# Kernel tuning notes

Hardware: AMD Instinct MI355X
Metric: run time of the kernel (lower is better)

The kernel has to match this reference:

```python
import jax, jax.numpy as jnp
from jax import lax
import numpy as np

B, T, IN, H, OUT = 8192, 512, 8, 64, 1


def setup_inputs() -> dict:
    key = jax.random.key(0)
    ks = jax.random.split(key, 7)
    s_ih = 1.0 / np.sqrt(H)
    # PyTorch LSTM param layout: gates stacked as [i, f, g, o] along dim 0
    W_ih = jax.random.uniform(ks[0], (4 * H, IN), jnp.float32, -s_ih, s_ih)
    W_hh = jax.random.uniform(ks[1], (4 * H, H), jnp.float32, -s_ih, s_ih)
    b_ih = jax.random.uniform(ks[2], (4 * H,), jnp.float32, -s_ih, s_ih)
    b_hh = jax.random.uniform(ks[3], (4 * H,), jnp.float32, -s_ih, s_ih)
    W_fc = jax.random.uniform(ks[4], (OUT, H), jnp.float32, -s_ih, s_ih)
    b_fc = jax.random.uniform(ks[5], (OUT,), jnp.float32, -s_ih, s_ih)
    x = jax.random.normal(ks[6], (B, T, IN), jnp.float32)
    return {"x": x, "W_ih": W_ih, "W_hh": W_hh, "b_ih": b_ih,
            "b_hh": b_hh, "W_fc": W_fc, "b_fc": b_fc}


def _lstm_last_h(x, W_ih, W_hh, b_ih, b_hh):
    # x: [B, T, IN] -> last hidden state [B, H]
    Bn = x.shape[0]
    Hn = W_hh.shape[1]
    b = b_ih + b_hh  # [4H]

    def step(carry, xt):
        h, c = carry  # [B, H] each
        gates = xt @ W_ih.T + h @ W_hh.T + b  # [B, 4H]
        i, f, g, o = jnp.split(gates, 4, axis=-1)
        i = jax.nn.sigmoid(i)
        f = jax.nn.sigmoid(f)
        g = jnp.tanh(g)
        o = jax.nn.sigmoid(o)
        c = f * c + i * g
        h = o * jnp.tanh(c)
        return (h, c), None

    h0 = jnp.zeros((Bn, Hn), x.dtype)
    c0 = jnp.zeros((Bn, Hn), x.dtype)
    (hT, _), _ = lax.scan(step, (h0, c0), jnp.swapaxes(x, 0, 1))  # scan over T
    return hT


def reference(x, W_ih, W_hh, b_ih, b_hh, W_fc, b_fc):
    hT = _lstm_last_h(x, W_ih, W_hh, b_ih, b_hh)  # [B, H]
    return hT @ W_fc.T + b_fc  # [B, OUT]
```

## Files before the change

kernel.cpp:

```cpp
#include <hip/hip_runtime.h>


typedef _Float16 f16_t;
typedef _Float16 half8 __attribute__((ext_vector_type(8)));
typedef __fp16 fp16x2 __attribute__((ext_vector_type(2)));
typedef float floatx2 __attribute__((ext_vector_type(2)));
typedef float floatx4 __attribute__((ext_vector_type(4)));

#define Bn 8192
#define Tn 512
#define INn 8
#define Hn 64
#define BT 16
#define CHUNK 16
#define NCHUNK (Tn / CHUNK)
#define HSTRIDE 72
#define XTSTRIDE 136

__device__ __forceinline__ floatx2 act_pair(float zi0, float zi1,
                                            float zf0, float zf1,
                                            float zg0, float zg1,
                                            float zo0, float zo1,
                                            floatx2& chat) {
  const floatx2 one  = {1.f, 1.f};
  const float  K2   = 2.8853900817779268f;
  const floatx2 K2v  = {K2, K2};
  const floatx2 mK2v = {-K2, -K2};
  const floatx2 clmp = {126.f, 126.f};
  floatx2 A = {__builtin_amdgcn_exp2f(zi0), __builtin_amdgcn_exp2f(zi1)};
  floatx2 G = {__builtin_amdgcn_exp2f(zg0), __builtin_amdgcn_exp2f(zg1)};
  floatx2 F = {__builtin_amdgcn_exp2f(zf0), __builtin_amdgcn_exp2f(zf1)};
  floatx2 O = {__builtin_amdgcn_exp2f(zo0), __builtin_amdgcn_exp2f(zo1)};
  floatx2 PA  = A + one;
  floatx2 PG  = G + one;
  floatx2 PF  = F + one;
  floatx2 PAG = PA * PG;
  floatx2 num = __builtin_elementwise_fma(G, K2v, mK2v) * PF;
  floatx2 s   = __builtin_elementwise_fma(chat, PAG, num);
  floatx2 P3  = PF * PAG;
  floatx2 R   = {__builtin_amdgcn_rcpf(P3.x), __builtin_amdgcn_rcpf(P3.y)};
  chat = __builtin_elementwise_min(s * R, clmp);
  floatx2 C2 = {__builtin_amdgcn_exp2f(chat.x), __builtin_amdgcn_exp2f(chat.y)};
  floatx2 P4 = (O + one) * (C2 + one);
  floatx2 Rh = {__builtin_amdgcn_rcpf(P4.x), __builtin_amdgcn_rcpf(P4.y)};
  return (C2 - one) * Rh;
}

__global__ __launch_bounds__(256, 2)
void lstm_fused(const float* __restrict__ xg,
                const float* __restrict__ W_ih,
                const float* __restrict__ W_hh,
                const float* __restrict__ b_ih,
                const float* __restrict__ b_hh,
                const float* __restrict__ W_fc,
                const float* __restrict__ b_fc,
                float* __restrict__ out)
{
  __shared__ alignas(16) f16_t hbuf[2][BT][HSTRIDE];
  __shared__ alignas(16) f16_t xlds[2][CHUNK][XTSTRIDE];

  const int tid   = threadIdx.x;
  const int wv    = tid >> 6;
  const int lane  = tid & 63;
  const int n     = lane & 15;
  const int q     = lane >> 4;
  const int bbase = blockIdx.x * BT;

  const float LOG2E = 1.4426950408889634f;

  half8 bf[4][3];
  #pragma unroll
  for (int g = 0; g < 4; ++g) {
    const float sc = (g == 2) ? (2.f * LOG2E) : (-LOG2E);
    const int C = g * 64 + wv * 16 + n;
    #pragma unroll
    for (int c = 0; c < 3; ++c) {
      half8 v;
      #pragma unroll
      for (int j = 0; j < 8; ++j) {
        const int k = c * 32 + q * 8 + j;
        float w = 0.f;
        if (k < Hn)            w = W_hh[C * Hn + k] * sc;
        else if (k < Hn + INn) w = W_ih[C * INn + (k - Hn)] * sc;
        v[j] = (f16_t)w;
      }
      bf[g][c] = v;
    }
  }

  const int u = wv * 16 + n;
  const float pb_i = -(b_ih[u]       + b_hh[u])       * LOG2E;
  const float pb_f = -(b_ih[64 + u]  + b_hh[64 + u])  * LOG2E;
  const float pb_g =  (b_ih[128 + u] + b_hh[128 + u]) * (2.f * LOG2E);
  const float pb_o = -(b_ih[192 + u] + b_hh[192 + u]) * LOG2E;
  const floatx4 bi  = {pb_i, pb_i, pb_i, pb_i};
  const floatx4 bfv = {pb_f, pb_f, pb_f, pb_f};
  const floatx4 bg  = {pb_g, pb_g, pb_g, pb_g};
  const floatx4 bo  = {pb_o, pb_o, pb_o, pb_o};

  for (int i = tid; i < BT * HSTRIDE; i += 256) ((f16_t*)hbuf[0])[i] = (f16_t)0.f;

  const int row_s = tid >> 4;
  const int tt_s  = tid & 15;
  const float* xps = xg + ((size_t)(bbase + row_s) * Tn + tt_s) * INn;

  float4 pa = *(const float4*)(xps);
  float4 pb2 = *(const float4*)(xps + 4);

  floatx2 chat01 = {0.f, 0.f};
  floatx2 chat23 = {0.f, 0.f};

  for (int ch = 0; ch < NCHUNK; ++ch) {
    union { half8 v; fp16x2 h2[4]; } P;
    P.h2[0] = __builtin_amdgcn_cvt_pkrtz(pa.x, pa.y);
    P.h2[1] = __builtin_amdgcn_cvt_pkrtz(pa.z, pa.w);
    P.h2[2] = __builtin_amdgcn_cvt_pkrtz(pb2.x, pb2.y);
    P.h2[3] = __builtin_amdgcn_cvt_pkrtz(pb2.z, pb2.w);
    *(half8*)&xlds[ch & 1][tt_s][row_s * 8] = P.v;
    __syncthreads();

    const int chn = (ch + 1 < NCHUNK) ? (ch + 1) : 0;
    pa  = *(const float4*)(xps + (size_t)chn * CHUNK * INn);
    pb2 = *(const float4*)(xps + (size_t)chn * CHUNK * INn + 4);

    #pragma unroll
    for (int tt = 0; tt < CHUNK; ++tt) {
      const int p  = tt & 1;
      const int pn = p ^ 1;

      const half8 a0 = *(const half8*)&hbuf[p][n][q * 8];
      const half8 a1 = *(const half8*)&hbuf[p][n][32 + q * 8];
      const half8 a2 = *(const half8*)&xlds[ch & 1][tt][n * 8];

      floatx4 ai = __builtin_amdgcn_mfma_f32_16x16x32_f16(a0, bf[0][0], bi, 0, 0, 0);
      ai = __builtin_amdgcn_mfma_f32_16x16x32_f16(a1, bf[0][1], ai, 0, 0, 0);
      ai = __builtin_amdgcn_mfma_f32_16x16x32_f16(a2, bf[0][2], ai, 0, 0, 0);
      floatx4 af = __builtin_amdgcn_mfma_f32_16x16x32_f16(a0, bf[1][0], bfv, 0, 0, 0);
      af = __builtin_amdgcn_mfma_f32_16x16x32_f16(a1, bf[1][1], af, 0, 0, 0);
      af = __builtin_amdgcn_mfma_f32_16x16x32_f16(a2, bf[1][2], af, 0, 0, 0);
      floatx4 ag = __builtin_amdgcn_mfma_f32_16x16x32_f16(a0, bf[2][0], bg, 0, 0, 0);
      ag = __builtin_amdgcn_mfma_f32_16x16x32_f16(a1, bf[2][1], ag, 0, 0, 0);
      ag = __builtin_amdgcn_mfma_f32_16x16x32_f16(a2, bf[2][2], ag, 0, 0, 0);
      floatx4 ao = __builtin_amdgcn_mfma_f32_16x16x32_f16(a0, bf[3][0], bo, 0, 0, 0);
      ao = __builtin_amdgcn_mfma_f32_16x16x32_f16(a1, bf[3][1], ao, 0, 0, 0);
      ao = __builtin_amdgcn_mfma_f32_16x16x32_f16(a2, bf[3][2], ao, 0, 0, 0);

      const floatx2 h01 = act_pair(ai[0], ai[1], af[0], af[1],
                                   ag[0], ag[1], ao[0], ao[1], chat01);
      const floatx2 h23 = act_pair(ai[2], ai[3], af[2], af[3],
                                   ag[2], ag[3], ao[2], ao[3], chat23);

      hbuf[pn][q * 4 + 0][u] = (f16_t)h01.x;
      hbuf[pn][q * 4 + 1][u] = (f16_t)h01.y;
      hbuf[pn][q * 4 + 2][u] = (f16_t)h23.x;
      hbuf[pn][q * 4 + 3][u] = (f16_t)h23.y;

      __syncthreads();
    }
  }

  if (tid < 64) {
    const int b = lane & 15;
    const int part = lane >> 4;
    float s = 0.f;
    #pragma unroll
    for (int k = 0; k < 16; ++k) {
      const int uu = part * 16 + k;
      s = __builtin_fmaf((float)hbuf[0][b][uu], W_fc[uu], s);
    }
    s += __shfl_down(s, 32);
    s += __shfl_down(s, 16);
    if (lane < 16) out[bbase + b] = s + b_fc[0];
  }
}

extern "C" void kernel_launch(void* const* d_in, const int* in_sizes, int n_in,
                              void* d_out, int out_size, void* d_ws, size_t ws_size,
                              hipStream_t stream) {
  const float* x    = (const float*)d_in[0];
  const float* W_ih = (const float*)d_in[1];
  const float* W_hh = (const float*)d_in[2];
  const float* b_ih = (const float*)d_in[3];
  const float* b_hh = (const float*)d_in[4];
  const float* W_fc = (const float*)d_in[5];
  const float* b_fc = (const float*)d_in[6];
  float* out = (float*)d_out;
  dim3 grid(Bn / BT), block(256);
  hipLaunchKernelGGL(lstm_fused, grid, block, 0, stream,
                     x, W_ih, W_hh, b_ih, b_hh, W_fc, b_fc, out);
}
```

Baseline: 448.3 us.

## Precompute next-step input projection off the recurrent critical path and remove per-chunk barrier

Result: slower. 462.3 us (+3.1%).

```diff
diff --git a/kernel.cpp b/kernel.cpp
--- a/kernel.cpp
+++ b/kernel.cpp
@@ -104,25 +104,31 @@
   const int tt_s  = tid & 15;
   const float* xps = xg + ((size_t)(bbase + row_s) * Tn + tt_s) * INn;
 
-  float4 pa = *(const float4*)(xps);
-  float4 pb2 = *(const float4*)(xps + 4);
+  {
+    float4 a  = *(const float4*)(xps);
+    float4 b2 = *(const float4*)(xps + 4);
+    union { half8 v; fp16x2 h2[4]; } P;
+    P.h2[0] = __builtin_amdgcn_cvt_pkrtz(a.x, a.y);
+    P.h2[1] = __builtin_amdgcn_cvt_pkrtz(a.z, a.w);
+    P.h2[2] = __builtin_amdgcn_cvt_pkrtz(b2.x, b2.y);
+    P.h2[3] = __builtin_amdgcn_cvt_pkrtz(b2.z, b2.w);
+    *(half8*)&xlds[0][tt_s][row_s * 8] = P.v;
+  }
+  float4 pa  = *(const float4*)(xps + CHUNK * INn);
+  float4 pb2 = *(const float4*)(xps + CHUNK * INn + 4);
+
+  __syncthreads();
+
+  half8 a2 = *(const half8*)&xlds[0][0][n * 8];
+  floatx4 xi  = __builtin_amdgcn_mfma_f32_16x16x32_f16(a2, bf[0][2], bi,  0, 0, 0);
+  floatx4 xfv = __builtin_amdgcn_mfma_f32_16x16x32_f16(a2, bf[1][2], bfv, 0, 0, 0);
+  floatx4 xgv = __builtin_amdgcn_mfma_f32_16x16x32_f16(a2, bf[2][2], bg,  0, 0, 0);
+  floatx4 xo  = __builtin_amdgcn_mfma_f32_16x16x32_f16(a2, bf[3][2], bo,  0, 0, 0);
 
   floatx2 chat01 = {0.f, 0.f};
   floatx2 chat23 = {0.f, 0.f};
 
   for (int ch = 0; ch < NCHUNK; ++ch) {
-    union { half8 v; fp16x2 h2[4]; } P;
-    P.h2[0] = __builtin_amdgcn_cvt_pkrtz(pa.x, pa.y);
-    P.h2[1] = __builtin_amdgcn_cvt_pkrtz(pa.z, pa.w);
-    P.h2[2] = __builtin_amdgcn_cvt_pkrtz(pb2.x, pb2.y);
-    P.h2[3] = __builtin_amdgcn_cvt_pkrtz(pb2.z, pb2.w);
-    *(half8*)&xlds[ch & 1][tt_s][row_s * 8] = P.v;
-    __syncthreads();
-
-    const int chn = (ch + 1 < NCHUNK) ? (ch + 1) : 0;
-    pa  = *(const float4*)(xps + (size_t)chn * CHUNK * INn);
-    pb2 = *(const float4*)(xps + (size_t)chn * CHUNK * INn + 4);
-
     #pragma unroll
     for (int tt = 0; tt < CHUNK; ++tt) {
       const int p  = tt & 1;
@@ -130,30 +136,48 @@
 
       const half8 a0 = *(const half8*)&hbuf[p][n][q * 8];
       const half8 a1 = *(const half8*)&hbuf[p][n][32 + q * 8];
-      const half8 a2 = *(const half8*)&xlds[ch & 1][tt][n * 8];
-
-      floatx4 ai = __builtin_amdgcn_mfma_f32_16x16x32_f16(a0, bf[0][0], bi, 0, 0, 0);
+
+      floatx4 ai = __builtin_amdgcn_mfma_f32_16x16x32_f16(a0, bf[0][0], xi,  0, 0, 0);
+      floatx4 af = __builtin_amdgcn_mfma_f32_16x16x32_f16(a0, bf[1][0], xfv, 0, 0, 0);
+      floatx4 ag = __builtin_amdgcn_mfma_f32_16x16x32_f16(a0, bf[2][0], xgv, 0, 0, 0);
+      floatx4 ao = __builtin_amdgcn_mfma_f32_16x16x32_f16(a0, bf[3][0], xo,  0, 0, 0);
       ai = __builtin_amdgcn_mfma_f32_16x16x32_f16(a1, bf[0][1], ai, 0, 0, 0);
-      ai = __builtin_amdgcn_mfma_f32_16x16x32_f16(a2, bf[0][2], ai, 0, 0, 0);
-      floatx4 af = __builtin_amdgcn_mfma_f32_16x16x32_f16(a0, bf[1][0], bfv, 0, 0, 0);
       af = __builtin_amdgcn_mfma_f32_16x16x32_f16(a1, bf[1][1], af, 0, 0, 0);
-      af = __builtin_amdgcn_mfma_f32_16x16x32_f16(a2, bf[1][2], af, 0, 0, 0);
-      floatx4 ag = __builtin_amdgcn_mfma_f32_16x16x32_f16(a0, bf[2][0], bg, 0, 0, 0);
       ag = __builtin_amdgcn_mfma_f32_16x16x32_f16(a1, bf[2][1], ag, 0, 0, 0);
-      ag = __builtin_amdgcn_mfma_f32_16x16x32_f16(a2, bf[2][2], ag, 0, 0, 0);
-      floatx4 ao = __builtin_amdgcn_mfma_f32_16x16x32_f16(a0, bf[3][0], bo, 0, 0, 0);
       ao = __builtin_amdgcn_mfma_f32_16x16x32_f16(a1, bf[3][1], ao, 0, 0, 0);
-      ao = __builtin_amdgcn_mfma_f32_16x16x32_f16(a2, bf[3][2], ao, 0, 0, 0);
+
+      if (tt == 0) {
+        union { half8 v; fp16x2 h2[4]; } P;
+        P.h2[0] = __builtin_amdgcn_cvt_pkrtz(pa.x, pa.y);
+        P.h2[1] = __builtin_amdgcn_cvt_pkrtz(pa.z, pa.w);
+        P.h2[2] = __builtin_amdgcn_cvt_pkrtz(pb2.x, pb2.y);
+        P.h2[3] = __builtin_amdgcn_cvt_pkrtz(pb2.z, pb2.w);
+        *(half8*)&xlds[(ch + 1) & 1][tt_s][row_s * 8] = P.v;
+      }
+      if (tt == 1) {
+        const int chn = (ch + 2 < NCHUNK) ? (ch + 2) : 0;
+        pa  = *(const float4*)(xps + (size_t)chn * CHUNK * INn);
+        pb2 = *(const float4*)(xps + (size_t)chn * CHUNK * INn + 4);
+      }
 
       const floatx2 h01 = act_pair(ai[0], ai[1], af[0], af[1],
                                    ag[0], ag[1], ao[0], ao[1], chat01);
+      hbuf[pn][q * 4 + 0][u] = (f16_t)h01.x;
+      hbuf[pn][q * 4 + 1][u] = (f16_t)h01.y;
       const floatx2 h23 = act_pair(ai[2], ai[3], af[2], af[3],
                                    ag[2], ag[3], ao[2], ao[3], chat23);
-
-      hbuf[pn][q * 4 + 0][u] = (f16_t)h01.x;
-      hbuf[pn][q * 4 + 1][u] = (f16_t)h01.y;
       hbuf[pn][q * 4 + 2][u] = (f16_t)h23.x;
       hbuf[pn][q * 4 + 3][u] = (f16_t)h23.y;
+
+      {
+        const int nbuf = (tt == CHUNK - 1) ? ((ch + 1) & 1) : (ch & 1);
+        const int ntt  = (tt + 1) & (CHUNK - 1);
+        a2 = *(const half8*)&xlds[nbuf][ntt][n * 8];
+        xi  = __builtin_amdgcn_mfma_f32_16x16x32_f16(a2, bf[0][2], bi,  0, 0, 0);
+        xfv = __builtin_amdgcn_mfma_f32_16x16x32_f16(a2, bf[1][2], bfv, 0, 0, 0);
+        xgv = __builtin_amdgcn_mfma_f32_16x16x32_f16(a2, bf[2][2], bg,  0, 0, 0);
+        xo  = __builtin_amdgcn_mfma_f32_16x16x32_f16(a2, bf[3][2], bo,  0, 0, 0);
+      }
 
       __syncthreads();
     }
```

## Interleave two batch tiles per block to overlap MFMA and activation chains

Applied to the files above, without the earlier changes.

Measured after the change: 517.5 us. +15.4%, slower.

```diff
diff --git a/kernel.cpp b/kernel.cpp
--- a/kernel.cpp
+++ b/kernel.cpp
@@ -12,6 +12,7 @@
 #define INn 8
 #define Hn 64
 #define BT 16
+#define NT 2
 #define CHUNK 16
 #define NCHUNK (Tn / CHUNK)
 #define HSTRIDE 72
@@ -46,7 +47,7 @@
   return (C2 - one) * Rh;
 }
 
-__global__ __launch_bounds__(256, 2)
+__global__ __launch_bounds__(256, 1)
 void lstm_fused(const float* __restrict__ xg,
                 const float* __restrict__ W_ih,
                 const float* __restrict__ W_hh,
@@ -56,15 +57,15 @@
                 const float* __restrict__ b_fc,
                 float* __restrict__ out)
 {
-  __shared__ alignas(16) f16_t hbuf[2][BT][HSTRIDE];
-  __shared__ alignas(16) f16_t xlds[2][CHUNK][XTSTRIDE];
+  __shared__ alignas(16) f16_t hbuf[NT][2][BT][HSTRIDE];
+  __shared__ alignas(16) f16_t xlds[NT][2][CHUNK][XTSTRIDE];
 
   const int tid   = threadIdx.x;
   const int wv    = tid >> 6;
   const int lane  = tid & 63;
   const int n     = lane & 15;
   const int q     = lane >> 4;
-  const int bbase = blockIdx.x * BT;
+  const int bbase = blockIdx.x * (BT * NT);
 
   const float LOG2E = 1.4426950408889634f;
 
@@ -98,79 +99,119 @@
   const floatx4 bg  = {pb_g, pb_g, pb_g, pb_g};
   const floatx4 bo  = {pb_o, pb_o, pb_o, pb_o};
 
-  for (int i = tid; i < BT * HSTRIDE; i += 256) ((f16_t*)hbuf[0])[i] = (f16_t)0.f;
+  for (int i = tid; i < NT * 2 * BT * HSTRIDE; i += 256)
+    ((f16_t*)hbuf)[i] = (f16_t)0.f;
 
   const int row_s = tid >> 4;
   const int tt_s  = tid & 15;
-  const float* xps = xg + ((size_t)(bbase + row_s) * Tn + tt_s) * INn;
-
-  float4 pa = *(const float4*)(xps);
-  float4 pb2 = *(const float4*)(xps + 4);
-
-  floatx2 chat01 = {0.f, 0.f};
-  floatx2 chat23 = {0.f, 0.f};
+  const float* xps0 = xg + ((size_t)(bbase + row_s) * Tn + tt_s) * INn;
+  const float* xps1 = xps0 + (size_t)BT * Tn * INn;
+
+  float4 pa0 = *(const float4*)(xps0);
+  float4 pb0 = *(const float4*)(xps0 + 4);
+  float4 pa1 = *(const float4*)(xps1);
+  float4 pb1 = *(const float4*)(xps1 + 4);
+
+  floatx2 chat01_0 = {0.f, 0.f};
+  floatx2 chat23_0 = {0.f, 0.f};
+  floatx2 chat01_1 = {0.f, 0.f};
+  floatx2 chat23_1 = {0.f, 0.f};
 
   for (int ch = 0; ch < NCHUNK; ++ch) {
-    union { half8 v; fp16x2 h2[4]; } P;
-    P.h2[0] = __builtin_amdgcn_cvt_pkrtz(pa.x, pa.y);
-    P.h2[1] = __builtin_amdgcn_cvt_pkrtz(pa.z, pa.w);
-    P.h2[2] = __builtin_amdgcn_cvt_pkrtz(pb2.x, pb2.y);
-    P.h2[3] = __builtin_amdgcn_cvt_pkrtz(pb2.z, pb2.w);
-    *(half8*)&xlds[ch & 1][tt_s][row_s * 8] = P.v;
+    {
+      union { half8 v; fp16x2 h2[4]; } P;
+      P.h2[0] = __builtin_amdgcn_cvt_pkrtz(pa0.x, pa0.y);
+      P.h2[1] = __builtin_amdgcn_cvt_pkrtz(pa0.z, pa0.w);
+      P.h2[2] = __builtin_amdgcn_cvt_pkrtz(pb0.x, pb0.y);
+      P.h2[3] = __builtin_amdgcn_cvt_pkrtz(pb0.z, pb0.w);
+      *(half8*)&xlds[0][ch & 1][tt_s][row_s * 8] = P.v;
+      P.h2[0] = __builtin_amdgcn_cvt_pkrtz(pa1.x, pa1.y);
+      P.h2[1] = __builtin_amdgcn_cvt_pkrtz(pa1.z, pa1.w);
+      P.h2[2] = __builtin_amdgcn_cvt_pkrtz(pb1.x, pb1.y);
+      P.h2[3] = __builtin_amdgcn_cvt_pkrtz(pb1.z, pb1.w);
+      *(half8*)&xlds[1][ch & 1][tt_s][row_s * 8] = P.v;
+    }
     __syncthreads();
 
     const int chn = (ch + 1 < NCHUNK) ? (ch + 1) : 0;
-    pa  = *(const float4*)(xps + (size_t)chn * CHUNK * INn);
-    pb2 = *(const float4*)(xps + (size_t)chn * CHUNK * INn + 4);
+    pa0 = *(const float4*)(xps0 + (size_t)chn * CHUNK * INn);
+    pb0 = *(const float4*)(xps0 + (size_t)chn * CHUNK * INn + 4);
+    pa1 = *(const float4*)(xps1 + (size_t)chn * CHUNK * INn);
+    pb1 = *(const float4*)(xps1 + (size_t)chn * CHUNK * INn + 4);
 
     #pragma unroll
     for (int tt = 0; tt < CHUNK; ++tt) {
       const int p  = tt & 1;
       const int pn = p ^ 1;
 
-      const half8 a0 = *(const half8*)&hbuf[p][n][q * 8];
-      const half8 a1 = *(const half8*)&hbuf[p][n][32 + q * 8];
-      const half8 a2 = *(const half8*)&xlds[ch & 1][tt][n * 8];
-
-      floatx4 ai = __builtin_amdgcn_mfma_f32_16x16x32_f16(a0, bf[0][0], bi, 0, 0, 0);
-      ai = __builtin_amdgcn_mfma_f32_16x16x32_f16(a1, bf[0][1], ai, 0, 0, 0);
-      ai = __builtin_amdgcn_mfma_f32_16x16x32_f16(a2, bf[0][2], ai, 0, 0, 0);
-      floatx4 af = __builtin_amdgcn_mfma_f32_16x16x32_f16(a0, bf[1][0], bfv, 0, 0, 0);
-      af = __builtin_amdgcn_mfma_f32_16x16x32_f16(a1, bf[1][1], af, 0, 0, 0);
-      af = __builtin_amdgcn_mfma_f32_16x16x32_f16(a2, bf[1][2], af, 0, 0, 0);
-      floatx4 ag = __builtin_amdgcn_mfma_f32_16x16x32_f16(a0, bf[2][0], bg, 0, 0, 0);
-      ag = __builtin_amdgcn_mfma_f32_16x16x32_f16(a1, bf[2][1], ag, 0, 0, 0);
-      ag = __builtin_amdgcn_mfma_f32_16x16x32_f16(a2, bf[2][2], ag, 0, 0, 0);
-      floatx4 ao = __builtin_amdgcn_mfma_f32_16x16x32_f16(a0, bf[3][0], bo, 0, 0, 0);
-      ao = __builtin_amdgcn_mfma_f32_16x16x32_f16(a1, bf[3][1], ao, 0, 0, 0);
-      ao = __builtin_amdgcn_mfma_f32_16x16x32_f16(a2, bf[3][2], ao, 0, 0, 0);
-
-      const floatx2 h01 = act_pair(ai[0], ai[1], af[0], af[1],
-                                   ag[0], ag[1], ao[0], ao[1], chat01);
-      const floatx2 h23 = act_pair(ai[2], ai[3], af[2], af[3],
-                                   ag[2], ag[3], ao[2], ao[3], chat23);
-
-      hbuf[pn][q * 4 + 0][u] = (f16_t)h01.x;
-      hbuf[pn][q * 4 + 1][u] = (f16_t)h01.y;
-      hbuf[pn][q * 4 + 2][u] = (f16_t)h23.x;
-      hbuf[pn][q * 4 + 3][u] = (f16_t)h23.y;
+      const half8 a00 = *(const half8*)&hbuf[0][p][n][q * 8];
+      const half8 a01 = *(const half8*)&hbuf[0][p][n][32 + q * 8];
+      const half8 a02 = *(const half8*)&xlds[0][ch & 1][tt][n * 8];
+      const half8 a10 = *(const half8*)&hbuf[1][p][n][q * 8];
+      const half8 a11 = *(const half8*)&hbuf[1][p][n][32 + q * 8];
+      const half8 a12 = *(const half8*)&xlds[1][ch & 1][tt][n * 8];
+
+      floatx4 ai0 = __builtin_amdgcn_mfma_f32_16x16x32_f16(a00, bf[0][0], bi,  0, 0, 0);
+      floatx4 af0 = __builtin_amdgcn_mfma_f32_16x16x32_f16(a00, bf[1][0], bfv, 0, 0, 0);
+      floatx4 ag0 = __builtin_amdgcn_mfma_f32_16x16x32_f16(a00, bf[2][0], bg,  0, 0, 0);
+      floatx4 ao0 = __builtin_amdgcn_mfma_f32_16x16x32_f16(a00, bf[3][0], bo,  0, 0, 0);
+      floatx4 ai1 = __builtin_amdgcn_mfma_f32_16x16x32_f16(a10, bf[0][0], bi,  0, 0, 0);
+      floatx4 af1 = __builtin_amdgcn_mfma_f32_16x16x32_f16(a10, bf[1][0], bfv, 0, 0, 0);
+      floatx4 ag1 = __builtin_amdgcn_mfma_f32_16x16x32_f16(a10, bf[2][0], bg,  0, 0, 0);
+      floatx4 ao1 = __builtin_amdgcn_mfma_f32_16x16x32_f16(a10, bf[3][0], bo,  0, 0, 0);
+
+      ai0 = __builtin_amdgcn_mfma_f32_16x16x32_f16(a01, bf[0][1], ai0, 0, 0, 0);
+      af0 = __builtin_amdgcn_mfma_f32_16x16x32_f16(a01, bf[1][1], af0, 0, 0, 0);
+      ag0 = __builtin_amdgcn_mfma_f32_16x16x32_f16(a01, bf[2][1], ag0, 0, 0, 0);
+      ao0 = __builtin_amdgcn_mfma_f32_16x16x32_f16(a01, bf[3][1], ao0, 0, 0, 0);
+      ai1 = __builtin_amdgcn_mfma_f32_16x16x32_f16(a11, bf[0][1], ai1, 0, 0, 0);
+      af1 = __builtin_amdgcn_mfma_f32_16x16x32_f16(a11, bf[1][1], af1, 0, 0, 0);
+      ag1 = __builtin_amdgcn_mfma_f32_16x16x32_f16(a11, bf[2][1], ag1, 0, 0, 0);
+      ao1 = __builtin_amdgcn_mfma_f32_16x16x32_f16(a11, bf[3][1], ao1, 0, 0, 0);
+
+      ai0 = __builtin_amdgcn_mfma_f32_16x16x32_f16(a02, bf[0][2], ai0, 0, 0, 0);
+      af0 = __builtin_amdgcn_mfma_f32_16x16x32_f16(a02, bf[1][2], af0, 0, 0, 0);
+      ag0 = __builtin_amdgcn_mfma_f32_16x16x32_f16(a02, bf[2][2], ag0, 0, 0, 0);
+      ao0 = __builtin_amdgcn_mfma_f32_16x16x32_f16(a02, bf[3][2], ao0, 0, 0, 0);
+      ai1 = __builtin_amdgcn_mfma_f32_16x16x32_f16(a12, bf[0][2], ai1, 0, 0, 0);
+      af1 = __builtin_amdgcn_mfma_f32_16x16x32_f16(a12, bf[1][2], af1, 0, 0, 0);
+      ag1 = __builtin_amdgcn_mfma_f32_16x16x32_f16(a12, bf[2][2], ag1, 0, 0, 0);
+      ao1 = __builtin_amdgcn_mfma_f32_16x16x32_f16(a12, bf[3][2], ao1, 0, 0, 0);
+
+      const floatx2 h01_0 = act_pair(ai0[0], ai0[1], af0[0], af0[1],
+                                     ag0[0], ag0[1], ao0[0], ao0[1], chat01_0);
+      hbuf[0][pn][q * 4 + 0][u] = (f16_t)h01_0.x;
+      hbuf[0][pn][q * 4 + 1][u] = (f16_t)h01_0.y;
+      const floatx2 h23_0 = act_pair(ai0[2], ai0[3], af0[2], af0[3],
+                                     ag0[2], ag0[3], ao0[2], ao0[3], chat23_0);
+      hbuf[0][pn][q * 4 + 2][u] = (f16_t)h23_0.x;
+      hbuf[0][pn][q * 4 + 3][u] = (f16_t)h23_0.y;
+      const floatx2 h01_1 = act_pair(ai1[0], ai1[1], af1[0], af1[1],
+                                     ag1[0], ag1[1], ao1[0], ao1[1], chat01_1);
+      hbuf[1][pn][q * 4 + 0][u] = (f16_t)h01_1.x;
+      hbuf[1][pn][q * 4 + 1][u] = (f16_t)h01_1.y;
+      const floatx2 h23_1 = act_pair(ai1[2], ai1[3], af1[2], af1[3],
+                                     ag1[2], ag1[3], ao1[2], ao1[3], chat23_1);
+      hbuf[1][pn][q * 4 + 2][u] = (f16_t)h23_1.x;
+      hbuf[1][pn][q * 4 + 3][u] = (f16_t)h23_1.y;
 
       __syncthreads();
     }
   }
 
-  if (tid < 64) {
+  if (wv < NT) {
+    const int tile = wv;
     const int b = lane & 15;
     const int part = lane >> 4;
     float s = 0.f;
     #pragma unroll
     for (int k = 0; k < 16; ++k) {
       const int uu = part * 16 + k;
-      s = __builtin_fmaf((float)hbuf[0][b][uu], W_fc[uu], s);
+      s = __builtin_fmaf((float)hbuf[tile][0][b][uu], W_fc[uu], s);
     }
     s += __shfl_down(s, 32);
     s += __shfl_down(s, 16);
-    if (lane < 16) out[bbase + b] = s + b_fc[0];
+    if (lane < 16) out[bbase + tile * BT + b] = s + b_fc[0];
   }
 }
 
@@ -185,7 +226,7 @@
   const float* W_fc = (const float*)d_in[5];
   const float* b_fc = (const float*)d_in[6];
   float* out = (float*)d_out;
-  dim3 grid(Bn / BT), block(256);
+  dim3 grid(Bn / (BT * NT)), block(256);
   hipLaunchKernelGGL(lstm_fused, grid, block, 0, stream,
                      x, W_ih, W_hh, b_ih, b_hh, W_fc, b_fc, out);
 }
```

## Transpose LSTM MFMA operands, use 16x16x16 for input term, vectorize h stores

Applied to the files above, without the earlier changes.

Measured after the change: 446.0 us. About the same (-0.5%).

```diff
diff --git a/kernel.cpp b/kernel.cpp
--- a/kernel.cpp
+++ b/kernel.cpp
@@ -3,6 +3,7 @@
 
 typedef _Float16 f16_t;
 typedef _Float16 half8 __attribute__((ext_vector_type(8)));
+typedef _Float16 half4 __attribute__((ext_vector_type(4)));
 typedef __fp16 fp16x2 __attribute__((ext_vector_type(2)));
 typedef float floatx2 __attribute__((ext_vector_type(2)));
 typedef float floatx4 __attribute__((ext_vector_type(4)));
@@ -15,7 +16,7 @@
 #define CHUNK 16
 #define NCHUNK (Tn / CHUNK)
 #define HSTRIDE 72
-#define XTSTRIDE 136
+#define XROW 24
 
 __device__ __forceinline__ floatx2 act_pair(float zi0, float zi1,
                                             float zf0, float zf1,
@@ -57,7 +58,7 @@
                 float* __restrict__ out)
 {
   __shared__ alignas(16) f16_t hbuf[2][BT][HSTRIDE];
-  __shared__ alignas(16) f16_t xlds[2][CHUNK][XTSTRIDE];
+  __shared__ alignas(16) f16_t xlds[2][CHUNK][BT][XROW];
 
   const int tid   = threadIdx.x;
   const int wv    = tid >> 6;
@@ -68,37 +69,45 @@
 
   const float LOG2E = 1.4426950408889634f;
 
-  half8 bf[4][3];
+  half8 bf[4][2];
+  half4 bfx[4];
   #pragma unroll
   for (int g = 0; g < 4; ++g) {
     const float sc = (g == 2) ? (2.f * LOG2E) : (-LOG2E);
     const int C = g * 64 + wv * 16 + n;
     #pragma unroll
-    for (int c = 0; c < 3; ++c) {
+    for (int c = 0; c < 2; ++c) {
       half8 v;
       #pragma unroll
       for (int j = 0; j < 8; ++j) {
         const int k = c * 32 + q * 8 + j;
-        float w = 0.f;
-        if (k < Hn)            w = W_hh[C * Hn + k] * sc;
-        else if (k < Hn + INn) w = W_ih[C * INn + (k - Hn)] * sc;
-        v[j] = (f16_t)w;
+        v[j] = (f16_t)(W_hh[C * Hn + k] * sc);
       }
       bf[g][c] = v;
     }
-  }
-
-  const int u = wv * 16 + n;
-  const float pb_i = -(b_ih[u]       + b_hh[u])       * LOG2E;
-  const float pb_f = -(b_ih[64 + u]  + b_hh[64 + u])  * LOG2E;
-  const float pb_g =  (b_ih[128 + u] + b_hh[128 + u]) * (2.f * LOG2E);
-  const float pb_o = -(b_ih[192 + u] + b_hh[192 + u]) * LOG2E;
-  const floatx4 bi  = {pb_i, pb_i, pb_i, pb_i};
-  const floatx4 bfv = {pb_f, pb_f, pb_f, pb_f};
-  const floatx4 bg  = {pb_g, pb_g, pb_g, pb_g};
-  const floatx4 bo  = {pb_o, pb_o, pb_o, pb_o};
+    half4 vx;
+    #pragma unroll
+    for (int j = 0; j < 4; ++j) {
+      const int k = q * 4 + j;
+      vx[j] = (f16_t)((k < INn) ? (W_ih[C * INn + k] * sc) : 0.f);
+    }
+    bfx[g] = vx;
+  }
+
+  const int u0 = wv * 16 + q * 4;
+  floatx4 bi, bfv, bg, bo;
+  #pragma unroll
+  for (int r = 0; r < 4; ++r) {
+    const int uu = u0 + r;
+    bi[r]  = -(b_ih[uu]        + b_hh[uu])        * LOG2E;
+    bfv[r] = -(b_ih[64 + uu]   + b_hh[64 + uu])   * LOG2E;
+    bg[r]  =  (b_ih[128 + uu]  + b_hh[128 + uu])  * (2.f * LOG2E);
+    bo[r]  = -(b_ih[192 + uu]  + b_hh[192 + uu])  * LOG2E;
+  }
 
   for (int i = tid; i < BT * HSTRIDE; i += 256) ((f16_t*)hbuf[0])[i] = (f16_t)0.f;
+  for (int i = tid; i < 2 * CHUNK * BT * XROW; i += 256) ((f16_t*)xlds)[i] = (f16_t)0.f;
+  __syncthreads();
 
   const int row_s = tid >> 4;
   const int tt_s  = tid & 15;
@@ -116,7 +125,7 @@
     P.h2[1] = __builtin_amdgcn_cvt_pkrtz(pa.z, pa.w);
     P.h2[2] = __builtin_amdgcn_cvt_pkrtz(pb2.x, pb2.y);
     P.h2[3] = __builtin_amdgcn_cvt_pkrtz(pb2.z, pb2.w);
-    *(half8*)&xlds[ch & 1][tt_s][row_s * 8] = P.v;
+    *(half8*)&xlds[ch & 1][tt_s][row_s][0] = P.v;
     __syncthreads();
 
     const int chn = (ch + 1 < NCHUNK) ? (ch + 1) : 0;
@@ -128,32 +137,32 @@
       const int p  = tt & 1;
       const int pn = p ^ 1;
 
-      const half8 a0 = *(const half8*)&hbuf[p][n][q * 8];
-      const half8 a1 = *(const half8*)&hbuf[p][n][32 + q * 8];
-      const half8 a2 = *(const half8*)&xlds[ch & 1][tt][n * 8];
-
-      floatx4 ai = __builtin_amdgcn_mfma_f32_16x16x32_f16(a0, bf[0][0], bi, 0, 0, 0);
-      ai = __builtin_amdgcn_mfma_f32_16x16x32_f16(a1, bf[0][1], ai, 0, 0, 0);
-      ai = __builtin_amdgcn_mfma_f32_16x16x32_f16(a2, bf[0][2], ai, 0, 0, 0);
-      floatx4 af = __builtin_amdgcn_mfma_f32_16x16x32_f16(a0, bf[1][0], bfv, 0, 0, 0);
-      af = __builtin_amdgcn_mfma_f32_16x16x32_f16(a1, bf[1][1], af, 0, 0, 0);
-      af = __builtin_amdgcn_mfma_f32_16x16x32_f16(a2, bf[1][2], af, 0, 0, 0);
-      floatx4 ag = __builtin_amdgcn_mfma_f32_16x16x32_f16(a0, bf[2][0], bg, 0, 0, 0);
-      ag = __builtin_amdgcn_mfma_f32_16x16x32_f16(a1, bf[2][1], ag, 0, 0, 0);
-      ag = __builtin_amdgcn_mfma_f32_16x16x32_f16(a2, bf[2][2], ag, 0, 0, 0);
-      floatx4 ao = __builtin_amdgcn_mfma_f32_16x16x32_f16(a0, bf[3][0], bo, 0, 0, 0);
-      ao = __builtin_amdgcn_mfma_f32_16x16x32_f16(a1, bf[3][1], ao, 0, 0, 0);
-      ao = __builtin_amdgcn_mfma_f32_16x16x32_f16(a2, bf[3][2], ao, 0, 0, 0);
+      const half8 b0 = *(const half8*)&hbuf[p][n][q * 8];
+      const half8 b1 = *(const half8*)&hbuf[p][n][32 + q * 8];
+      const half4 bx = *(const half4*)&xlds[ch & 1][tt][n][q * 4];
+
+      floatx4 ai = __builtin_amdgcn_mfma_f32_16x16x32_f16(bf[0][0], b0, bi,  0, 0, 0);
+      floatx4 af = __builtin_amdgcn_mfma_f32_16x16x32_f16(bf[1][0], b0, bfv, 0, 0, 0);
+      floatx4 ag = __builtin_amdgcn_mfma_f32_16x16x32_f16(bf[2][0], b0, bg,  0, 0, 0);
+      floatx4 ao = __builtin_amdgcn_mfma_f32_16x16x32_f16(bf[3][0], b0, bo,  0, 0, 0);
+      ai = __builtin_amdgcn_mfma_f32_16x16x32_f16(bf[0][1], b1, ai, 0, 0, 0);
+      af = __builtin_amdgcn_mfma_f32_16x16x32_f16(bf[1][1], b1, af, 0, 0, 0);
+      ag = __builtin_amdgcn_mfma_f32_16x16x32_f16(bf[2][1], b1, ag, 0, 0, 0);
+      ao = __builtin_amdgcn_mfma_f32_16x16x32_f16(bf[3][1], b1, ao, 0, 0, 0);
+      ai = __builtin_amdgcn_mfma_f32_16x16x16f16(bfx[0], bx, ai, 0, 0, 0);
+      af = __builtin_amdgcn_mfma_f32_16x16x16f16(bfx[1], bx, af, 0, 0, 0);
+      ag = __builtin_amdgcn_mfma_f32_16x16x16f16(bfx[2], bx, ag, 0, 0, 0);
+      ao = __builtin_amdgcn_mfma_f32_16x16x16f16(bfx[3], bx, ao, 0, 0, 0);
 
       const floatx2 h01 = act_pair(ai[0], ai[1], af[0], af[1],
                                    ag[0], ag[1], ao[0], ao[1], chat01);
       const floatx2 h23 = act_pair(ai[2], ai[3], af[2], af[3],
                                    ag[2], ag[3], ao[2], ao[3], chat23);
 
-      hbuf[pn][q * 4 + 0][u] = (f16_t)h01.x;
-      hbuf[pn][q * 4 + 1][u] = (f16_t)h01.y;
-      hbuf[pn][q * 4 + 2][u] = (f16_t)h23.x;
-      hbuf[pn][q * 4 + 3][u] = (f16_t)h23.y;
+      union { half4 v; fp16x2 h2[2]; } Wq;
+      Wq.h2[0] = __builtin_amdgcn_cvt_pkrtz(h01.x, h01.y);
+      Wq.h2[1] = __builtin_amdgcn_cvt_pkrtz(h23.x, h23.y);
+      *(half4*)&hbuf[pn][n][u0] = Wq.v;
 
       __syncthreads();
     }
```
